# Kernel tuning notes

Measured on AMD Instinct MI355X. Metric: run time of the kernel, lower is better.

The kernel has to match this reference:

```python
import jax, jax.numpy as jnp
import numpy as np

ALPHA_REC = 2.0
ALPHA_SMOOTH = 3.0


def setup_inputs() -> dict:
    key = jax.random.key(0)
    k1, k2 = jax.random.split(key)
    B, C, T, J = 2048, 3, 300, 25
    inputs = jax.random.normal(k1, (B, C, T, J), dtype=jnp.float32)
    targets = jax.random.normal(k2, (B, C, T, J), dtype=jnp.float32)
    return {"inputs": inputs, "targets": targets}


def _smooth_loss(inputs, targets):
    # torch permute(0,3,2,1): [B, C, T, J] -> [B, J, T, C]
    x = jnp.transpose(inputs, (0, 3, 2, 1))
    t = jnp.transpose(targets, (0, 3, 2, 1))
    J, T = x.shape[1], x.shape[2]
    # Faithful to source quirk: x[:, i, j] - x[:, i, j+1] ** 2 (next frame squared,
    # NOT squared difference), summed over j = 0..T-2.  Shapes: [B, J, C].
    sx = jnp.sum(x[:, :, :-1] - jnp.square(x[:, :, 1:]), axis=2)
    st = jnp.sum(t[:, :, :-1] - jnp.square(t[:, :, 1:]), axis=2)
    # Loop over i = 0..J-2 only (last joint excluded in the source).
    total = jnp.sum(jnp.abs(sx - st)[:, : J - 1], axis=1)  # [B, C]
    loss = jnp.sqrt(total) / (J * T)
    return jnp.mean(loss)


def reference(inputs, targets):
    loss_rec = jnp.mean(jnp.square(inputs - targets))
    loss_smooth = _smooth_loss(inputs, targets)
    return ALPHA_REC * loss_rec + ALPHA_SMOOTH * loss_smooth
```

## Files before the change

kernel.cpp:

```cpp
#include <hip/hip_runtime.h>
#include <math.h>

constexpr int B_ = 2048, C_ = 3, T_ = 300, J_ = 25;
constexpr int SLAB  = T_ * J_;
constexpr int NBC   = B_ * C_;
constexpr int NQ    = SLAB / 4;
constexpr int NCHUNK = (NQ + 63) / 64;

__device__ __forceinline__ void gl_lds16(const float* g, float* l) {
  __builtin_amdgcn_global_load_lds(
      (const __attribute__((address_space(1))) void*)g,
      (__attribute__((address_space(3))) void*)l, 16, 0, 0);
}

__global__ __launch_bounds__(256) void slab_kernel(
    const float* __restrict__ gin, const float* __restrict__ gtg,
    float* __restrict__ rec_part, float* __restrict__ sm_part) {
  __shared__ __align__(16) float s_in[SLAB];
  __shared__ __align__(16) float s_tg[SLAB];
  __shared__ float s_part[256];
  __shared__ float s_red[4];

  const int tid  = threadIdx.x;
  const int lane = tid & 63;
  const int wave = tid >> 6;
  const size_t base = (size_t)blockIdx.x * SLAB;
  const float* in = gin + base;
  const float* tg = gtg + base;

  for (int c = wave; c < NCHUNK; c += 4) {
    const int e = c * 64 + lane;
    if (e < NQ) {
      gl_lds16(in + e * 4, s_in + c * 256);
      gl_lds16(tg + e * 4, s_tg + c * 256);
    }
  }
  __builtin_amdgcn_s_waitcnt(0);
  __syncthreads();

  float racc = 0.f;
  const float4* v_in = (const float4*)s_in;
  const float4* v_tg = (const float4*)s_tg;
  for (int i = tid; i < NQ; i += 256) {
    float4 a = v_in[i], b = v_tg[i];
    float d0 = a.x - b.x, d1 = a.y - b.y, d2 = a.z - b.z, d3 = a.w - b.w;
    racc += d0 * d0 + d1 * d1 + d2 * d2 + d3 * d3;
  }

  if (tid < 250) {
    const int j  = tid % 25;
    const int s  = tid / 25;
    const int t0 = s * 30;
    float p = 0.f;
    #pragma unroll
    for (int k = 0; k < 30; ++k) {
      const int t = t0 + k;
      const float x = s_in[t * 25 + j];
      const float y = s_tg[t * 25 + j];
      if (t < T_ - 1) p += x - y;
      if (t > 0)      p += (y - x) * (y + x);
    }
    s_part[s * 25 + j] = p;
  }

  #pragma unroll
  for (int off = 32; off > 0; off >>= 1) racc += __shfl_down(racc, off, 64);
  if (lane == 0) s_red[wave] = racc;
  __syncthreads();

  if (wave == 0) {
    float aval = 0.f;
    if (lane < J_ - 1) {
      float dx = 0.f;
      #pragma unroll
      for (int s = 0; s < 10; ++s) dx += s_part[s * 25 + lane];
      aval = fabsf(dx);
    }
    #pragma unroll
    for (int off = 32; off > 0; off >>= 1) aval += __shfl_down(aval, off, 64);
    if (lane == 0) {
      rec_part[blockIdx.x] = s_red[0] + s_red[1] + s_red[2] + s_red[3];
      sm_part[blockIdx.x]  = sqrtf(aval);
    }
  }
}

__global__ __launch_bounds__(256) void finalize_kernel(
    const float* __restrict__ rec_part, const float* __restrict__ sm_part,
    float* __restrict__ out) {
  const int tid  = threadIdx.x;
  const int lane = tid & 63;
  const int wave = tid >> 6;
  double r = 0.0, s = 0.0;
  for (int i = tid; i < NBC; i += 256) {
    r += (double)rec_part[i];
    s += (double)sm_part[i];
  }
  #pragma unroll
  for (int off = 32; off > 0; off >>= 1) {
    r += __shfl_down(r, off, 64);
    s += __shfl_down(s, off, 64);
  }
  __shared__ double sr[4], ss[4];
  if (lane == 0) { sr[wave] = r; ss[wave] = s; }
  __syncthreads();
  if (tid == 0) {
    const double rt = sr[0] + sr[1] + sr[2] + sr[3];
    const double st = ss[0] + ss[1] + ss[2] + ss[3];
    const double loss_rec    = rt / (double)((long long)B_ * C_ * T_ * J_);
    const double loss_smooth = (st / (double)NBC) / (double)(J_ * T_);
    out[0] = (float)(2.0 * loss_rec + 3.0 * loss_smooth);
  }
}

extern "C" void kernel_launch(void* const* d_in, const int* in_sizes, int n_in,
                              void* d_out, int out_size, void* d_ws, size_t ws_size,
                              hipStream_t stream) {
  const float* in = (const float*)d_in[0];
  const float* tg = (const float*)d_in[1];
  float* rec_part = (float*)d_ws;
  float* sm_part  = rec_part + NBC;
  slab_kernel<<<NBC, 256, 0, stream>>>(in, tg, rec_part, sm_part);
  finalize_kernel<<<1, 256, 0, stream>>>(rec_part, sm_part, (float*)d_out);
}
```

Baseline: 364.7 us.

## Replace LDS slab staging with direct vectorized global loads and column atomics

Removes the full-slab copy of inputs and targets into shared memory. Each thread now streams float4 values directly from global memory and computes the reconstruction and smoothness partials in one pass. Because the thread stride is a multiple of the joint count, each thread's lanes stay on fixed joints, and per-joint sums are combined with shared-memory atomics. This frees roughly 60KB of LDS per block, which raises occupancy and memory parallelism, at the cost of a few LDS atomics per thread.

After: 369.5 us. Within noise of the previous version (+1.3%).

```diff
diff --git a/kernel.cpp b/kernel.cpp
--- a/kernel.cpp
+++ b/kernel.cpp
@@ -2,80 +2,61 @@
 #include <math.h>
 
 constexpr int B_ = 2048, C_ = 3, T_ = 300, J_ = 25;
-constexpr int SLAB  = T_ * J_;
-constexpr int NBC   = B_ * C_;
-constexpr int NQ    = SLAB / 4;
-constexpr int NCHUNK = (NQ + 63) / 64;
+constexpr int SLAB = T_ * J_;
+constexpr int NBC  = B_ * C_;
 
-__device__ __forceinline__ void gl_lds16(const float* g, float* l) {
-  __builtin_amdgcn_global_load_lds(
-      (const __attribute__((address_space(1))) void*)g,
-      (__attribute__((address_space(3))) void*)l, 16, 0, 0);
-}
-
-__global__ __launch_bounds__(256) void slab_kernel(
+__global__ __launch_bounds__(256) void fused_kernel(
     const float* __restrict__ gin, const float* __restrict__ gtg,
     float* __restrict__ rec_part, float* __restrict__ sm_part) {
-  __shared__ __align__(16) float s_in[SLAB];
-  __shared__ __align__(16) float s_tg[SLAB];
-  __shared__ float s_part[256];
+  __shared__ float s_col[J_];
   __shared__ float s_red[4];
 
   const int tid  = threadIdx.x;
   const int lane = tid & 63;
   const int wave = tid >> 6;
+
+  if (tid < J_) s_col[tid] = 0.f;
+  __syncthreads();
+
   const size_t base = (size_t)blockIdx.x * SLAB;
   const float* in = gin + base;
   const float* tg = gtg + base;
 
-  for (int c = wave; c < NCHUNK; c += 4) {
-    const int e = c * 64 + lane;
-    if (e < NQ) {
-      gl_lds16(in + e * 4, s_in + c * 256);
-      gl_lds16(tg + e * 4, s_tg + c * 256);
-    }
-  }
-  __builtin_amdgcn_s_waitcnt(0);
-  __syncthreads();
-
-  float racc = 0.f;
-  const float4* v_in = (const float4*)s_in;
-  const float4* v_tg = (const float4*)s_tg;
-  for (int i = tid; i < NQ; i += 256) {
-    float4 a = v_in[i], b = v_tg[i];
-    float d0 = a.x - b.x, d1 = a.y - b.y, d2 = a.z - b.z, d3 = a.w - b.w;
-    racc += d0 * d0 + d1 * d1 + d2 * d2 + d3 * d3;
-  }
+  float rec = 0.f;
+  float p0 = 0.f, p1 = 0.f, p2 = 0.f, p3 = 0.f;
+  const int e0 = tid * 4;
 
   if (tid < 250) {
-    const int j  = tid % 25;
-    const int s  = tid / 25;
-    const int t0 = s * 30;
-    float p = 0.f;
     #pragma unroll
-    for (int k = 0; k < 30; ++k) {
-      const int t = t0 + k;
-      const float x = s_in[t * 25 + j];
-      const float y = s_tg[t * 25 + j];
-      if (t < T_ - 1) p += x - y;
-      if (t > 0)      p += (y - x) * (y + x);
+    for (int it = 0; it < 8; ++it) {
+      const int e = it * 1000 + e0;
+      if (e < SLAB) {
+        const float4 x = *(const float4*)(in + e);
+        const float4 y = *(const float4*)(tg + e);
+        { float d = x.x - y.x, s = x.x + y.x; rec += d * d;
+          p0 += (e     < 7475 ? d : 0.f) - (e     >= 25 ? d * s : 0.f); }
+        { float d = x.y - y.y, s = x.y + y.y; rec += d * d;
+          p1 += (e + 1 < 7475 ? d : 0.f) - (e + 1 >= 25 ? d * s : 0.f); }
+        { float d = x.z - y.z, s = x.z + y.z; rec += d * d;
+          p2 += (e + 2 < 7475 ? d : 0.f) - (e + 2 >= 25 ? d * s : 0.f); }
+        { float d = x.w - y.w, s = x.w + y.w; rec += d * d;
+          p3 += (e + 3 < 7475 ? d : 0.f) - (e + 3 >= 25 ? d * s : 0.f); }
+      }
     }
-    s_part[s * 25 + j] = p;
+    const int j0 = (tid * 4) % 25;
+    atomicAdd(&s_col[j0],            p0);
+    atomicAdd(&s_col[(j0 + 1) % 25], p1);
+    atomicAdd(&s_col[(j0 + 2) % 25], p2);
+    atomicAdd(&s_col[(j0 + 3) % 25], p3);
   }
 
   #pragma unroll
-  for (int off = 32; off > 0; off >>= 1) racc += __shfl_down(racc, off, 64);
-  if (lane == 0) s_red[wave] = racc;
+  for (int off = 32; off > 0; off >>= 1) rec += __shfl_down(rec, off, 64);
+  if (lane == 0) s_red[wave] = rec;
   __syncthreads();
 
   if (wave == 0) {
-    float aval = 0.f;
-    if (lane < J_ - 1) {
-      float dx = 0.f;
-      #pragma unroll
-      for (int s = 0; s < 10; ++s) dx += s_part[s * 25 + lane];
-      aval = fabsf(dx);
-    }
+    float aval = (lane < J_ - 1) ? fabsf(s_col[lane]) : 0.f;
     #pragma unroll
     for (int off = 32; off > 0; off >>= 1) aval += __shfl_down(aval, off, 64);
     if (lane == 0) {
@@ -120,6 +101,6 @@
   const float* tg = (const float*)d_in[1];
   float* rec_part = (float*)d_ws;
   float* sm_part  = rec_part + NBC;
-  slab_kernel<<<NBC, 256, 0, stream>>>(in, tg, rec_part, sm_part);
+  fused_kernel<<<NBC, 256, 0, stream>>>(in, tg, rec_part, sm_part);
   finalize_kernel<<<1, 256, 0, stream>>>(rec_part, sm_part, (float*)d_out);
 }
```
